# Optimization experiments

Measured on AMD Instinct MI355X. Metric: run time of the kernel, lower is better.

Reference implementation:

```python
import jax, jax.numpy as jnp
import numpy as np

E = 200000     # number of edge-level cells
NADJ = 3200000 # directed up / down adjacency entries (avg degree 16)
F = 64         # input feature dim (== hidden so all layers share dims)
H = 64         # hidden dim
L = 3          # num_layers
B = 64         # number of graphs in batch
C = 10         # num_classes


def setup_inputs() -> dict:
    key = jax.random.key(0)
    ks = jax.random.split(key, 12)
    x = jax.random.normal(ks[0], (E, F), dtype=jnp.float32)
    up_index = jax.random.randint(ks[1], (2, NADJ), 0, E, dtype=jnp.int32)
    up_orient = 2.0 * jax.random.randint(ks[2], (NADJ,), 0, 2).astype(jnp.float32) - 1.0
    down_index = jax.random.randint(ks[3], (2, NADJ), 0, E, dtype=jnp.int32)
    down_orient = 2.0 * jax.random.randint(ks[4], (NADJ,), 0, 2).astype(jnp.float32) - 1.0
    batch = jnp.sort(jax.random.randint(ks[5], (E,), 0, B, dtype=jnp.int32))
    s = 1.0 / np.sqrt(H)
    W_up = jax.random.uniform(ks[6], (L, H, H), minval=-s, maxval=s, dtype=jnp.float32)
    W_down = jax.random.uniform(ks[7], (L, H, H), minval=-s, maxval=s, dtype=jnp.float32)
    W_self = jax.random.uniform(ks[8], (L, H, H), minval=-s, maxval=s, dtype=jnp.float32)
    lin1_w = jax.random.uniform(ks[9], (H, H), minval=-s, maxval=s, dtype=jnp.float32)
    lin1_b = jnp.zeros((H,), jnp.float32)
    lin2_w = jax.random.uniform(ks[10], (C, H), minval=-s, maxval=s, dtype=jnp.float32)
    lin2_b = jnp.zeros((C,), jnp.float32)
    return {"x": x, "up_index": up_index, "up_orient": up_orient,
            "down_index": down_index, "down_orient": down_orient, "batch": batch,
            "W_up": W_up, "W_down": W_down, "W_self": W_self,
            "lin1_w": lin1_w, "lin1_b": lin1_b, "lin2_w": lin2_w, "lin2_b": lin2_b}


def reference(x, up_index, up_orient, down_index, down_orient, batch,
              W_up, W_down, W_self, lin1_w, lin1_b, lin2_w, lin2_b):
    up_src, up_dst = up_index[0], up_index[1]      # message flows src -> dst
    dn_src, dn_dst = down_index[0], down_index[1]
    h = x
    for l in range(L):
        # sign-weighted gather + scatter-sum over upper/lower adjacency
        m_up = jax.ops.segment_sum(h[up_src] * up_orient[:, None], up_dst, num_segments=E)
        m_dn = jax.ops.segment_sum(h[dn_src] * down_orient[:, None], dn_dst, num_segments=E)
        # OrientedConv: act(update_nn(x) + update_up_nn(agg_up) + update_down_nn(agg_down))
        h = jnp.tanh(h @ W_self[l].T + m_up @ W_up[l].T + m_dn @ W_down[l].T)
    # orientation-invariant readout: abs then per-graph segment sum
    pooled = jax.ops.segment_sum(jnp.abs(h), batch, num_segments=B)  # [B, H]
    z = jax.nn.relu(pooled @ lin1_w.T + lin1_b)
    # dropout(p=0.0, eval) is identity
    return z @ lin2_w.T + lin2_b  # [B, C]
```

## Files before the change

kernel.cpp:

```cpp
#include <hip/hip_runtime.h>
#include <hip/hip_bf16.h>

#define H64 64
typedef float float4a __attribute__((ext_vector_type(4)));
typedef float f32x4  __attribute__((ext_vector_type(4)));
typedef short bf16x8 __attribute__((ext_vector_type(8)));

__device__ __forceinline__ unsigned short f2bf(float x) {
    unsigned b = __float_as_uint(x);
    unsigned r = (b + 0x7fffu + ((b >> 16) & 1u)) >> 16;
    return (unsigned short)r;
}

#define SCAN_B 256

#define RPB       512
#define RPB_SH    9
#define NBKT_MAX  1024
#define R1_CHUNK  8192
#define BC_CHUNK  16384

__global__ __launch_bounds__(256) void bcount_kernel(
    const int* __restrict__ up_dst, const int* __restrict__ dn_dst,
    int* __restrict__ bktcnt, int nadj, int E, int nbkt)
{
    __shared__ int lc[NBKT_MAX];
    int t = threadIdx.x;
    for (int i = t; i < nbkt; i += 256) lc[i] = 0;
    __syncthreads();
    long long base = (long long)blockIdx.x * BC_CHUNK;
    long long total = 2LL * nadj;
    for (int i = 0; i < BC_CHUNK / 256; ++i) {
        long long g = base + i * 256 + t;
        if (g < total) {
            int dst2 = (g < nadj) ? up_dst[(int)g] : E + dn_dst[(int)(g - nadj)];
            atomicAdd(&lc[dst2 >> RPB_SH], 1);
        }
    }
    __syncthreads();
    for (int i = t; i < nbkt; i += 256) {
        int c = lc[i];
        if (c) atomicAdd(&bktcnt[i], c);
    }
}

__global__ __launch_bounds__(256) void bscan_kernel(
    const int* __restrict__ bktcnt, int* __restrict__ bstart, int* __restrict__ gcur,
    int nbkt, int total)
{
    __shared__ int s[SCAN_B];
    int t = threadIdx.x;
    int i0 = t * 4;
    int v0 = (i0     < nbkt) ? bktcnt[i0]     : 0;
    int v1 = (i0 + 1 < nbkt) ? bktcnt[i0 + 1] : 0;
    int v2 = (i0 + 2 < nbkt) ? bktcnt[i0 + 2] : 0;
    int v3 = (i0 + 3 < nbkt) ? bktcnt[i0 + 3] : 0;
    int tsum = v0 + v1 + v2 + v3;
    s[t] = tsum; __syncthreads();
    for (int off = 1; off < SCAN_B; off <<= 1) {
        int add = (t >= off) ? s[t - off] : 0;
        int cur = s[t];
        __syncthreads();
        s[t] = cur + add;
        __syncthreads();
    }
    int excl = s[t] - tsum;
    if (i0     < nbkt) { bstart[i0]     = excl;                gcur[i0]     = excl; }
    if (i0 + 1 < nbkt) { bstart[i0 + 1] = excl + v0;           gcur[i0 + 1] = excl + v0; }
    if (i0 + 2 < nbkt) { bstart[i0 + 2] = excl + v0 + v1;      gcur[i0 + 2] = excl + v0 + v1; }
    if (i0 + 3 < nbkt) { bstart[i0 + 3] = excl + v0 + v1 + v2; gcur[i0 + 3] = excl + v0 + v1 + v2; }
    if (t == 0) bstart[nbkt] = total;
}

__global__ __launch_bounds__(256) void bin_kernel(
    const int* __restrict__ up_index, const float* __restrict__ up_orient,
    const int* __restrict__ dn_index, const float* __restrict__ dn_orient,
    int* __restrict__ gcur, unsigned* __restrict__ binned,
    int nadj, int E, int nbkt)
{
    __shared__ unsigned sval[R1_CHUNK];
    __shared__ unsigned short sbkt[R1_CHUNK];
    __shared__ int lcnt[NBKT_MAX];
    __shared__ int goff[NBKT_MAX];
    __shared__ int lrank[NBKT_MAX];

    int t = threadIdx.x;
    for (int b = t; b < nbkt; b += 256) lcnt[b] = 0;
    __syncthreads();

    long long base = (long long)blockIdx.x * R1_CHUNK;
    int total = 2 * nadj;
    #pragma unroll 4
    for (int i = 0; i < R1_CHUNK / 256; ++i) {
        long long g = base + i * 256 + t;
        int li = i * 256 + t;
        if (g < total) {
            int src, dst2; float orient;
            if (g < nadj) {
                int e = (int)g;
                src = up_index[e]; dst2 = up_index[nadj + e]; orient = up_orient[e];
            } else {
                int e = (int)(g - nadj);
                src = dn_index[e]; dst2 = E + dn_index[nadj + e]; orient = dn_orient[e];
            }
            unsigned v = ((unsigned)src << RPB_SH) | (unsigned)(dst2 & (RPB - 1))
                       | (orient < 0.f ? 0x80000000u : 0u);
            int bk = dst2 >> RPB_SH;
            sval[li] = v;
            sbkt[li] = (unsigned short)bk;
            atomicAdd(&lcnt[bk], 1);
        } else {
            sbkt[li] = 0xFFFFu;
        }
    }
    __syncthreads();
    for (int b = t; b < nbkt; b += 256) {
        int c = lcnt[b];
        lrank[b] = 0;
        if (c > 0) goff[b] = atomicAdd(&gcur[b], c);
    }
    __syncthreads();
    #pragma unroll 4
    for (int i = 0; i < R1_CHUNK / 256; ++i) {
        int li = i * 256 + t;
        unsigned short bk = sbkt[li];
        if (bk != 0xFFFFu) {
            int r = atomicAdd(&lrank[bk], 1);
            binned[goff[bk] + r] = sval[li];
        }
    }
}

__global__ __launch_bounds__(256) void csr_fill2_kernel(
    const unsigned* __restrict__ binned, const int* __restrict__ bstart,
    int* __restrict__ end2, unsigned* __restrict__ packed2, int n2)
{
    __shared__ int lh[RPB];
    __shared__ int lcur[RPB];
    __shared__ int s[SCAN_B];
    int b = blockIdx.x;
    int t = threadIdx.x;
    int s0 = bstart[b], s1 = bstart[b + 1];
    int dbase = b << RPB_SH;

    for (int i = t; i < RPB; i += 256) lh[i] = 0;
    __syncthreads();
    for (int i = s0 + t; i < s1; i += 256) {
        unsigned v = binned[i];
        atomicAdd(&lh[v & (RPB - 1)], 1);
    }
    __syncthreads();

    int i0 = t * 2;
    int c0 = lh[i0], c1 = lh[i0 + 1];
    int tsum = c0 + c1;
    s[t] = tsum; __syncthreads();
    for (int off = 1; off < SCAN_B; off <<= 1) {
        int add = (t >= off) ? s[t - off] : 0;
        int cur = s[t];
        __syncthreads();
        s[t] = cur + add;
        __syncthreads();
    }
    int excl = s[t] - tsum;
    lcur[i0]     = excl;
    lcur[i0 + 1] = excl + c0;
    int gd = dbase + i0;
    if (gd     < n2) end2[gd]     = s0 + excl + c0;
    if (gd + 1 < n2) end2[gd + 1] = s0 + excl + tsum;
    __syncthreads();

    for (int i = s0 + t; i < s1; i += 256) {
        unsigned v = binned[i];
        int d = (int)(v & (RPB - 1));
        int p = atomicAdd(&lcur[d], 1);
        packed2[s0 + p] = (v & 0x80000000u) | ((v >> RPB_SH) & 0x1FFFFFu);
    }
}

#define SCAN_TILE 1024

__global__ __launch_bounds__(256) void hist2_kernel(
    const int* __restrict__ up_dst, const int* __restrict__ dn_dst,
    int* __restrict__ deg2, int nadj, int E)
{
    int g = blockIdx.x * 256 + threadIdx.x;
    if (g < nadj) {
        atomicAdd(&deg2[up_dst[g]], 1);
    } else {
        int e = g - nadj;
        if (e < nadj) atomicAdd(&deg2[E + dn_dst[e]], 1);
    }
}

__global__ __launch_bounds__(256) void scan_partial(
    const int* __restrict__ deg, int* __restrict__ bsums, int n)
{
    __shared__ int s[SCAN_B];
    int t = threadIdx.x;
    int i0 = blockIdx.x * SCAN_TILE + t * 4;
    int sum = 0;
    if (i0 + 3 < n) {
        int4 v = *(const int4*)(deg + i0);
        sum = v.x + v.y + v.z + v.w;
    } else {
        for (int k = 0; k < 4; ++k) if (i0 + k < n) sum += deg[i0 + k];
    }
    s[t] = sum; __syncthreads();
    for (int off = 128; off > 0; off >>= 1) {
        if (t < off) s[t] += s[t + off];
        __syncthreads();
    }
    if (t == 0) bsums[blockIdx.x] = s[0];
}

__global__ __launch_bounds__(256) void scan_bsums_k(int* bsums, int nblk)
{
    __shared__ int s[SCAN_B];
    int t = threadIdx.x;
    int i0 = t * 4;
    int v0 = 0, v1 = 0, v2 = 0, v3 = 0;
    if (i0     < nblk) v0 = bsums[i0];
    if (i0 + 1 < nblk) v1 = bsums[i0 + 1];
    if (i0 + 2 < nblk) v2 = bsums[i0 + 2];
    if (i0 + 3 < nblk) v3 = bsums[i0 + 3];
    int tsum = v0 + v1 + v2 + v3;
    s[t] = tsum; __syncthreads();
    for (int off = 1; off < SCAN_B; off <<= 1) {
        int add = (t >= off) ? s[t - off] : 0;
        int cur = s[t];
        __syncthreads();
        s[t] = cur + add;
        __syncthreads();
    }
    int excl = s[t] - tsum;
    if (i0     < nblk) bsums[i0]     = excl;
    if (i0 + 1 < nblk) bsums[i0 + 1] = excl + v0;
    if (i0 + 2 < nblk) bsums[i0 + 2] = excl + v0 + v1;
    if (i0 + 3 < nblk) bsums[i0 + 3] = excl + v0 + v1 + v2;
}

__global__ __launch_bounds__(256) void scan_final(
    const int* __restrict__ deg, const int* __restrict__ bsums,
    int* __restrict__ outx, int n)
{
    __shared__ int s[SCAN_B];
    int t = threadIdx.x;
    int i0 = blockIdx.x * SCAN_TILE + t * 4;
    int v0 = 0, v1 = 0, v2 = 0, v3 = 0;
    if (i0 + 3 < n) {
        int4 v = *(const int4*)(deg + i0);
        v0 = v.x; v1 = v.y; v2 = v.z; v3 = v.w;
    } else {
        if (i0     < n) v0 = deg[i0];
        if (i0 + 1 < n) v1 = deg[i0 + 1];
        if (i0 + 2 < n) v2 = deg[i0 + 2];
        if (i0 + 3 < n) v3 = deg[i0 + 3];
    }
    int tsum = v0 + v1 + v2 + v3;
    s[t] = tsum; __syncthreads();
    for (int off = 1; off < SCAN_B; off <<= 1) {
        int add = (t >= off) ? s[t - off] : 0;
        int cur = s[t];
        __syncthreads();
        s[t] = cur + add;
        __syncthreads();
    }
    int excl = s[t] - tsum;
    int base = bsums[blockIdx.x] + excl;
    if (i0     < n) outx[i0]     = base;
    if (i0 + 1 < n) outx[i0 + 1] = base + v0;
    if (i0 + 2 < n) outx[i0 + 2] = base + v0 + v1;
    if (i0 + 3 < n) outx[i0 + 3] = base + v0 + v1 + v2;
}

__global__ __launch_bounds__(256) void reorder2_kernel(
    const int* __restrict__ up_index, const float* __restrict__ up_orient,
    const int* __restrict__ dn_index, const float* __restrict__ dn_orient,
    int* __restrict__ end2, unsigned* __restrict__ packed2, int nadj, int E)
{
    int g = blockIdx.x * 256 + threadIdx.x;
    if (g < nadj) {
        int src = up_index[g];
        int dst = up_index[nadj + g];
        int p = atomicAdd(&end2[dst], 1);
        packed2[p] = (unsigned)src | (up_orient[g] < 0.f ? 0x80000000u : 0u);
    } else {
        int e = g - nadj;
        if (e < nadj) {
            int src = dn_index[e];
            int dst = dn_index[nadj + e];
            int p = atomicAdd(&end2[E + dst], 1);
            packed2[p] = (unsigned)src | (dn_orient[e] < 0.f ? 0x80000000u : 0u);
        }
    }
}

__global__ __launch_bounds__(256) void conv_bf16_kernel(
    const float* __restrict__ x, unsigned short* __restrict__ hb, size_t n)
{
    size_t i = ((size_t)blockIdx.x * 256 + threadIdx.x) * 4;
    if (i + 3 < n) {
        float4a v = *(const float4a*)(x + i);
        uint2 o;
        o.x = (unsigned)f2bf(v[0]) | ((unsigned)f2bf(v[1]) << 16);
        o.y = (unsigned)f2bf(v[2]) | ((unsigned)f2bf(v[3]) << 16);
        *(uint2*)(hb + i) = o;
    } else {
        for (size_t k = i; k < n; ++k) hb[k] = f2bf(x[k]);
    }
}

__global__ __launch_bounds__(256) void convW_kernel(
    const float* __restrict__ Ws, const float* __restrict__ Wu,
    const float* __restrict__ Wd, unsigned short* __restrict__ Wb, int L)
{
    int i = blockIdx.x * 256 + threadIdx.x;
    int total = L * 3 * 4096;
    if (i >= total) return;
    int l = i / (3 * 4096);
    int m = (i / 4096) % 3;
    int r = i & 4095;
    const float* src = (m == 0) ? Ws : ((m == 1) ? Wu : Wd);
    Wb[i] = f2bf(src[l * 4096 + r]);
}

__device__ __forceinline__ void seg_sum2_slow(
    const unsigned* __restrict__ hb32, const unsigned* __restrict__ packed2,
    int s0, int s1, unsigned fp, int g, int lane, float& r0, float& r1)
{
    float a0 = 0.f, a1 = 0.f;
    for (int b = s0; b < s1; b += 64) {
        int cnt = min(64, s1 - b);
        unsigned pk = (lane < cnt) ? packed2[b + lane] : 0u;
        for (int n = 0; n < cnt; n += 2) {
            int idx = n + g;
            unsigned pe = __shfl(pk, min(idx, cnt - 1));
            float sgn = (idx < cnt) ? (((int)pe < 0) ? -1.f : 1.f) : 0.f;
            unsigned u = hb32[(pe << 5) + fp];
            a0 = fmaf(__uint_as_float(u << 16),         sgn, a0);
            a1 = fmaf(__uint_as_float(u & 0xFFFF0000u), sgn, a1);
        }
    }
    r0 = a0; r1 = a1;
}

__global__ __launch_bounds__(256) void gather_kernel(
    const unsigned* __restrict__ hb32,
    const int* __restrict__ end2, const unsigned* __restrict__ packed2,
    unsigned* __restrict__ mup32, unsigned* __restrict__ mdn32, int E)
{
    int dst = (int)((blockIdx.x * 256u + threadIdx.x) >> 6);
    if (dst >= E) return;
    int lane = threadIdx.x & 63;
    int g  = lane >> 5;
    unsigned fp = lane & 31;

    int s0U = (dst == 0) ? 0 : end2[dst - 1];
    int s1U = end2[dst];
    int s0D = end2[E + dst - 1];
    int s1D = end2[E + dst];
    int cntU = s1U - s0U, cntD = s1D - s0D;

    float u0, u1, d0, d1;
    if (cntU <= 64 && cntD <= 64) {
        int limU = max(cntU - 1, 0), limD = max(cntD - 1, 0);
        unsigned pkU = (cntU > 0) ? packed2[s0U + min(lane, limU)] : 0u;
        unsigned pkD = (cntD > 0) ? packed2[s0D + min(lane, limD)] : 0u;
        float a0 = 0.f, a1 = 0.f, b0 = 0.f, b1 = 0.f;
        int nmax = max(cntU, cntD);
        for (int n = 0; n < nmax; n += 8) {
            unsigned pU[4], pD[4], vU[4], vD[4];
            float sU[4], sD[4];
            #pragma unroll
            for (int t = 0; t < 4; ++t) {
                int idx = n + 2 * t + g;
                pU[t] = __shfl(pkU, min(idx, limU));
                pD[t] = __shfl(pkD, min(idx, limD));
                sU[t] = (idx < cntU) ? (((int)pU[t] < 0) ? -1.f : 1.f) : 0.f;
                sD[t] = (idx < cntD) ? (((int)pD[t] < 0) ? -1.f : 1.f) : 0.f;
            }
            #pragma unroll
            for (int t = 0; t < 4; ++t) vU[t] = hb32[(pU[t] << 5) + fp];
            #pragma unroll
            for (int t = 0; t < 4; ++t) vD[t] = hb32[(pD[t] << 5) + fp];
            #pragma unroll
            for (int t = 0; t < 4; ++t) {
                a0 = fmaf(__uint_as_float(vU[t] << 16),         sU[t], a0);
                a1 = fmaf(__uint_as_float(vU[t] & 0xFFFF0000u), sU[t], a1);
                b0 = fmaf(__uint_as_float(vD[t] << 16),         sD[t], b0);
                b1 = fmaf(__uint_as_float(vD[t] & 0xFFFF0000u), sD[t], b1);
            }
        }
        u0 = a0; u1 = a1; d0 = b0; d1 = b1;
    } else {
        seg_sum2_slow(hb32, packed2, s0U, s1U, fp, g, lane, u0, u1);
        seg_sum2_slow(hb32, packed2, s0D, s1D, fp, g, lane, d0, d1);
    }

    u0 += __shfl_xor(u0, 32); u1 += __shfl_xor(u1, 32);
    d0 += __shfl_xor(d0, 32); d1 += __shfl_xor(d1, 32);

    unsigned valU = (unsigned)f2bf(u0) | ((unsigned)f2bf(u1) << 16);
    unsigned valD = (unsigned)f2bf(d0) | ((unsigned)f2bf(d1) << 16);
    unsigned* ptr = g ? mdn32 : mup32;
    ptr[(size_t)dst * 32 + fp] = g ? valD : valU;
}

__global__ __launch_bounds__(256) void gemm_tanh_mfma(
    const unsigned short* __restrict__ hbin,
    const unsigned short* __restrict__ mupb, const unsigned short* __restrict__ mdnb,
    const unsigned short* __restrict__ Wb,
    unsigned short* __restrict__ hbout, int E, int nblk16)
{
    int wid  = (blockIdx.x * 256 + threadIdx.x) >> 6;
    if (wid >= nblk16) return;
    int lane = threadIdx.x & 63;
    int lg = lane >> 4;
    int lr = lane & 15;

    bf16x8 bfr[3][4][2];
    #pragma unroll
    for (int m = 0; m < 3; ++m)
        #pragma unroll
        for (int jt = 0; jt < 4; ++jt)
            #pragma unroll
            for (int ks = 0; ks < 2; ++ks)
                bfr[m][jt][ks] = *(const bf16x8*)(Wb + m * 4096 + (jt * 16 + lr) * 64 + ks * 32 + lg * 8);

    int base = wid * 16;
    int arow = base + lr;
    bool ok = (arow < E);
    size_t aoff = (size_t)arow * H64 + lg * 8;

    bf16x8 afr[3][2];
    bf16x8 zz = {0, 0, 0, 0, 0, 0, 0, 0};
    #pragma unroll
    for (int ks = 0; ks < 2; ++ks) {
        afr[0][ks] = ok ? *(const bf16x8*)(hbin + aoff + ks * 32) : zz;
        afr[1][ks] = ok ? *(const bf16x8*)(mupb + aoff + ks * 32) : zz;
        afr[2][ks] = ok ? *(const bf16x8*)(mdnb + aoff + ks * 32) : zz;
    }

    f32x4 acc[4];
    #pragma unroll
    for (int jt = 0; jt < 4; ++jt) acc[jt] = (f32x4){0.f, 0.f, 0.f, 0.f};

    #pragma unroll
    for (int m = 0; m < 3; ++m)
        #pragma unroll
        for (int ks = 0; ks < 2; ++ks)
            #pragma unroll
            for (int jt = 0; jt < 4; ++jt)
                acc[jt] = __builtin_amdgcn_mfma_f32_16x16x32_bf16(
                    afr[m][ks], bfr[m][jt][ks], acc[jt], 0, 0, 0);

    #pragma unroll
    for (int jt = 0; jt < 4; ++jt) {
        #pragma unroll
        for (int reg = 0; reg < 4; ++reg) {
            int row = base + lg * 4 + reg;
            if (row < E) {
                float v = acc[jt][reg];
                float e2 = __expf(2.f * v);
                float val = 1.f - 2.f / (e2 + 1.f);
                hbout[(size_t)row * H64 + jt * 16 + lr] = f2bf(val);
            }
        }
    }
}

#define ROWS_PER_WAVE 64
__global__ __launch_bounds__(256) void pool_kernel(
    const unsigned short* __restrict__ hb, const int* __restrict__ batch,
    float* __restrict__ pooled, int E)
{
    int wave = (int)((blockIdx.x * 256 + threadIdx.x) >> 6);
    int j = threadIdx.x & 63;
    int row0 = wave * ROWS_PER_WAVE;
    if (row0 >= E) return;
    int row1 = min(row0 + ROWS_PER_WAVE, E);

    int cur = batch[row0];
    float acc = 0.f;
    for (int i = row0; i < row1; ++i) {
        int b = batch[i];
        if (b != cur) {
            atomicAdd(&pooled[(size_t)cur * H64 + j], acc);
            acc = 0.f;
            cur = b;
        }
        unsigned u = hb[(size_t)i * H64 + j];
        acc += fabsf(__uint_as_float(u << 16));
    }
    atomicAdd(&pooled[(size_t)cur * H64 + j], acc);
}

__global__ __launch_bounds__(64) void head_kernel(
    const float* __restrict__ pooled,
    const float* __restrict__ lin1_w, const float* __restrict__ lin1_b,
    const float* __restrict__ lin2_w, const float* __restrict__ lin2_b,
    float* __restrict__ out, int C)
{
    __shared__ float p[64];
    __shared__ float z[64];
    int b = blockIdx.x;
    int t = threadIdx.x;

    p[t] = pooled[(size_t)b * H64 + t];
    __syncthreads();

    float acc = lin1_b[t];
    #pragma unroll
    for (int k = 0; k < 64; ++k) acc += p[k] * lin1_w[t * 64 + k];
    z[t] = fmaxf(acc, 0.f);
    __syncthreads();

    if (t < C) {
        float o = lin2_b[t];
        #pragma unroll
        for (int k = 0; k < 64; ++k) o += z[k] * lin2_w[t * 64 + k];
        out[(size_t)b * C + t] = o;
    }
}

extern "C" void kernel_launch(void* const* d_in, const int* in_sizes, int n_in,
                              void* d_out, int out_size, void* d_ws, size_t ws_size,
                              hipStream_t stream)
{
    const float* x          = (const float*)d_in[0];
    const int*   up_index   = (const int*)  d_in[1];
    const float* up_orient  = (const float*)d_in[2];
    const int*   down_index = (const int*)  d_in[3];
    const float* down_orient= (const float*)d_in[4];
    const int*   batch      = (const int*)  d_in[5];
    const float* W_up       = (const float*)d_in[6];
    const float* W_down     = (const float*)d_in[7];
    const float* W_self     = (const float*)d_in[8];
    const float* lin1_w     = (const float*)d_in[9];
    const float* lin1_b     = (const float*)d_in[10];
    const float* lin2_w     = (const float*)d_in[11];
    const float* lin2_b     = (const float*)d_in[12];
    float* out = (float*)d_out;

    const int E    = in_sizes[0] / H64;
    const int NADJ = in_sizes[1] / 2;
    const int C    = in_sizes[11] / H64;
    const int B    = out_size / C;
    const int L    = in_sizes[6] / (H64 * H64);

    unsigned short* hb      = (unsigned short*)d_ws;
    unsigned short* mupb    = hb   + (size_t)E * H64;
    unsigned short* mdnb    = mupb + (size_t)E * H64;
    float*          pooled  = (float*)(mdnb + (size_t)E * H64);
    int*            end2    = (int*)(pooled + (size_t)B * H64);
    int*            deg2    = end2 + (size_t)2 * E;
    int*            bsums   = deg2 + (size_t)2 * E;
    int*            bktcnt  = bsums + 1024;
    int*            gcur    = bktcnt + NBKT_MAX;
    int*            bstart  = gcur + NBKT_MAX;
    unsigned short* Wb      = (unsigned short*)(bstart + NBKT_MAX + 1);
    unsigned*       packed2 = (unsigned*)(Wb + (size_t)L * 3 * 4096);
    unsigned*       binned  = packed2 + (size_t)2 * NADJ;

    const int n2    = 2 * E;
    const int nbkt  = (n2 + RPB - 1) >> RPB_SH;
    const int total = 2 * NADJ;
    const int gather_blocks = (int)(((long long)E * 64 + 255) / 256);
    const int conv_blocks   = (int)(((long long)E * H64 / 4 + 255) / 256);
    const int nblk16        = (E + 15) / 16;
    const int gemm_blocks   = (nblk16 + 3) / 4;
    const int convw_blocks  = (L * 3 * 4096 + 255) / 256;
    const int pool_waves    = (E + ROWS_PER_WAVE - 1) / ROWS_PER_WAVE;
    const int pool_blocks   = (pool_waves + 3) / 4;

    if (nbkt <= NBKT_MAX) {
        const int bc_blocks = (total + BC_CHUNK - 1) / BC_CHUNK;
        const int r1_blocks = (total + R1_CHUNK - 1) / R1_CHUNK;
        hipMemsetAsync(bktcnt, 0, (size_t)NBKT_MAX * sizeof(int), stream);
        bcount_kernel<<<bc_blocks, 256, 0, stream>>>(up_index + NADJ, down_index + NADJ,
                                                     bktcnt, NADJ, E, nbkt);
        bscan_kernel<<<1, 256, 0, stream>>>(bktcnt, bstart, gcur, nbkt, total);
        bin_kernel<<<r1_blocks, 256, 0, stream>>>(up_index, up_orient, down_index, down_orient,
                                                  gcur, binned, NADJ, E, nbkt);
        csr_fill2_kernel<<<nbkt, 256, 0, stream>>>(binned, bstart, end2, packed2, n2);
    } else {
        const int both_blocks = (total + 255) / 256;
        const int nscan = (n2 + SCAN_TILE - 1) / SCAN_TILE;
        hipMemsetAsync(deg2, 0, (size_t)n2 * sizeof(int), stream);
        hist2_kernel<<<both_blocks, 256, 0, stream>>>(up_index + NADJ, down_index + NADJ, deg2, NADJ, E);
        scan_partial<<<nscan, 256, 0, stream>>>(deg2, bsums, n2);
        scan_bsums_k<<<1, 256, 0, stream>>>(bsums, nscan);
        scan_final<<<nscan, 256, 0, stream>>>(deg2, bsums, end2, n2);
        reorder2_kernel<<<both_blocks, 256, 0, stream>>>(up_index, up_orient, down_index, down_orient,
                                                         end2, packed2, NADJ, E);
    }

    conv_bf16_kernel<<<conv_blocks, 256, 0, stream>>>(x, hb, (size_t)E * H64);
    convW_kernel<<<convw_blocks, 256, 0, stream>>>(W_self, W_up, W_down, Wb, L);

    for (int l = 0; l < L; ++l) {
        gather_kernel<<<gather_blocks, 256, 0, stream>>>(
            (const unsigned*)hb, end2, packed2,
            (unsigned*)mupb, (unsigned*)mdnb, E);
        gemm_tanh_mfma<<<gemm_blocks, 256, 0, stream>>>(
            hb, mupb, mdnb, Wb + (size_t)l * 3 * 4096, hb, E, nblk16);
    }

    hipMemsetAsync(pooled, 0, (size_t)B * H64 * sizeof(float), stream);
    pool_kernel<<<pool_blocks, 256, 0, stream>>>(hb, batch, pooled, E);
    head_kernel<<<B, 64, 0, stream>>>(pooled, lin1_w, lin1_b, lin2_w, lin2_b, out, C);
}
```

Baseline: 731.5 us.

## Fuse conversion kernels, split gather tail loops, stream GEMM weight loads

Merges the activation and weight bf16 conversion kernels into one launch, saving a kernel launch. The gather loop now runs paired up/down iterations only up to the smaller count and finishes the rest in separate single-direction loops, so the direction with fewer neighbours no longer issues wasted clamped loads. The MFMA GEMM loads the A and B fragments per matrix inside the loop instead of preloading all of them into registers, which lowers register pressure and may raise occupancy but puts the weight loads closer to their use.

```diff
diff --git a/kernel.cpp b/kernel.cpp
--- a/kernel.cpp
+++ b/kernel.cpp
@@ -296,33 +296,33 @@
     }
 }
 
-__global__ __launch_bounds__(256) void conv_bf16_kernel(
-    const float* __restrict__ x, unsigned short* __restrict__ hb, size_t n)
-{
-    size_t i = ((size_t)blockIdx.x * 256 + threadIdx.x) * 4;
-    if (i + 3 < n) {
-        float4a v = *(const float4a*)(x + i);
-        uint2 o;
-        o.x = (unsigned)f2bf(v[0]) | ((unsigned)f2bf(v[1]) << 16);
-        o.y = (unsigned)f2bf(v[2]) | ((unsigned)f2bf(v[3]) << 16);
-        *(uint2*)(hb + i) = o;
-    } else {
-        for (size_t k = i; k < n; ++k) hb[k] = f2bf(x[k]);
-    }
-}
-
-__global__ __launch_bounds__(256) void convW_kernel(
+__global__ __launch_bounds__(256) void conv_all_kernel(
+    const float* __restrict__ x, unsigned short* __restrict__ hb, size_t n,
+    int conv_blocks,
     const float* __restrict__ Ws, const float* __restrict__ Wu,
     const float* __restrict__ Wd, unsigned short* __restrict__ Wb, int L)
 {
-    int i = blockIdx.x * 256 + threadIdx.x;
-    int total = L * 3 * 4096;
-    if (i >= total) return;
-    int l = i / (3 * 4096);
-    int m = (i / 4096) % 3;
-    int r = i & 4095;
-    const float* src = (m == 0) ? Ws : ((m == 1) ? Wu : Wd);
-    Wb[i] = f2bf(src[l * 4096 + r]);
+    if (blockIdx.x < (unsigned)conv_blocks) {
+        size_t i = ((size_t)blockIdx.x * 256 + threadIdx.x) * 4;
+        if (i + 3 < n) {
+            float4a v = *(const float4a*)(x + i);
+            uint2 o;
+            o.x = (unsigned)f2bf(v[0]) | ((unsigned)f2bf(v[1]) << 16);
+            o.y = (unsigned)f2bf(v[2]) | ((unsigned)f2bf(v[3]) << 16);
+            *(uint2*)(hb + i) = o;
+        } else {
+            for (size_t k = i; k < n; ++k) hb[k] = f2bf(x[k]);
+        }
+    } else {
+        int i = (blockIdx.x - conv_blocks) * 256 + threadIdx.x;
+        int total = L * 3 * 4096;
+        if (i >= total) return;
+        int l = i / (3 * 4096);
+        int m = (i / 4096) % 3;
+        int r = i & 4095;
+        const float* src = (m == 0) ? Ws : ((m == 1) ? Wu : Wd);
+        Wb[i] = f2bf(src[l * 4096 + r]);
+    }
 }
 
 __device__ __forceinline__ void seg_sum2_slow(
@@ -368,8 +368,9 @@
         unsigned pkU = (cntU > 0) ? packed2[s0U + min(lane, limU)] : 0u;
         unsigned pkD = (cntD > 0) ? packed2[s0D + min(lane, limD)] : 0u;
         float a0 = 0.f, a1 = 0.f, b0 = 0.f, b1 = 0.f;
-        int nmax = max(cntU, cntD);
-        for (int n = 0; n < nmax; n += 8) {
+        int nmin = min(cntU, cntD);
+        int n = 0;
+        for (; n < nmin; n += 8) {
             unsigned pU[4], pD[4], vU[4], vD[4];
             float sU[4], sD[4];
             #pragma unroll
@@ -392,6 +393,38 @@
                 b1 = fmaf(__uint_as_float(vD[t] & 0xFFFF0000u), sD[t], b1);
             }
         }
+        for (int q = n; q < cntU; q += 8) {
+            unsigned p[4], v[4]; float sg[4];
+            #pragma unroll
+            for (int t = 0; t < 4; ++t) {
+                int idx = q + 2 * t + g;
+                p[t] = __shfl(pkU, min(idx, limU));
+                sg[t] = (idx < cntU) ? (((int)p[t] < 0) ? -1.f : 1.f) : 0.f;
+            }
+            #pragma unroll
+            for (int t = 0; t < 4; ++t) v[t] = hb32[(p[t] << 5) + fp];
+            #pragma unroll
+            for (int t = 0; t < 4; ++t) {
+                a0 = fmaf(__uint_as_float(v[t] << 16),         sg[t], a0);
+                a1 = fmaf(__uint_as_float(v[t] & 0xFFFF0000u), sg[t], a1);
+            }
+        }
+        for (int q = n; q < cntD; q += 8) {
+            unsigned p[4], v[4]; float sg[4];
+            #pragma unroll
+            for (int t = 0; t < 4; ++t) {
+                int idx = q + 2 * t + g;
+                p[t] = __shfl(pkD, min(idx, limD));
+                sg[t] = (idx < cntD) ? (((int)p[t] < 0) ? -1.f : 1.f) : 0.f;
+            }
+            #pragma unroll
+            for (int t = 0; t < 4; ++t) v[t] = hb32[(p[t] << 5) + fp];
+            #pragma unroll
+            for (int t = 0; t < 4; ++t) {
+                b0 = fmaf(__uint_as_float(v[t] << 16),         sg[t], b0);
+                b1 = fmaf(__uint_as_float(v[t] & 0xFFFF0000u), sg[t], b1);
+            }
+        }
         u0 = a0; u1 = a1; d0 = b0; d1 = b1;
     } else {
         seg_sum2_slow(hb32, packed2, s0U, s1U, fp, g, lane, u0, u1);
@@ -419,41 +452,30 @@
     int lg = lane >> 4;
     int lr = lane & 15;
 
-    bf16x8 bfr[3][4][2];
-    #pragma unroll
-    for (int m = 0; m < 3; ++m)
-        #pragma unroll
-        for (int jt = 0; jt < 4; ++jt)
-            #pragma unroll
-            for (int ks = 0; ks < 2; ++ks)
-                bfr[m][jt][ks] = *(const bf16x8*)(Wb + m * 4096 + (jt * 16 + lr) * 64 + ks * 32 + lg * 8);
-
     int base = wid * 16;
     int arow = base + lr;
     bool ok = (arow < E);
     size_t aoff = (size_t)arow * H64 + lg * 8;
 
-    bf16x8 afr[3][2];
-    bf16x8 zz = {0, 0, 0, 0, 0, 0, 0, 0};
-    #pragma unroll
-    for (int ks = 0; ks < 2; ++ks) {
-        afr[0][ks] = ok ? *(const bf16x8*)(hbin + aoff + ks * 32) : zz;
-        afr[1][ks] = ok ? *(const bf16x8*)(mupb + aoff + ks * 32) : zz;
-        afr[2][ks] = ok ? *(const bf16x8*)(mdnb + aoff + ks * 32) : zz;
-    }
-
     f32x4 acc[4];
     #pragma unroll
     for (int jt = 0; jt < 4; ++jt) acc[jt] = (f32x4){0.f, 0.f, 0.f, 0.f};
 
+    bf16x8 zz = {0, 0, 0, 0, 0, 0, 0, 0};
     #pragma unroll
-    for (int m = 0; m < 3; ++m)
+    for (int m = 0; m < 3; ++m) {
+        const unsigned short* src = (m == 0) ? hbin : ((m == 1) ? mupb : mdnb);
+        bf16x8 a0 = ok ? *(const bf16x8*)(src + aoff)      : zz;
+        bf16x8 a1 = ok ? *(const bf16x8*)(src + aoff + 32) : zz;
+        const unsigned short* wbase = Wb + m * 4096 + lr * 64 + lg * 8;
         #pragma unroll
-        for (int ks = 0; ks < 2; ++ks)
-            #pragma unroll
-            for (int jt = 0; jt < 4; ++jt)
-                acc[jt] = __builtin_amdgcn_mfma_f32_16x16x32_bf16(
-                    afr[m][ks], bfr[m][jt][ks], acc[jt], 0, 0, 0);
+        for (int jt = 0; jt < 4; ++jt) {
+            bf16x8 b0 = *(const bf16x8*)(wbase + jt * 1024);
+            bf16x8 b1 = *(const bf16x8*)(wbase + jt * 1024 + 32);
+            acc[jt] = __builtin_amdgcn_mfma_f32_16x16x32_bf16(a0, b0, acc[jt], 0, 0, 0);
+            acc[jt] = __builtin_amdgcn_mfma_f32_16x16x32_bf16(a1, b1, acc[jt], 0, 0, 0);
+        }
+    }
 
     #pragma unroll
     for (int jt = 0; jt < 4; ++jt) {
@@ -568,9 +590,9 @@
     const int total = 2 * NADJ;
     const int gather_blocks = (int)(((long long)E * 64 + 255) / 256);
     const int conv_blocks   = (int)(((long long)E * H64 / 4 + 255) / 256);
+    const int convw_blocks  = (L * 3 * 4096 + 255) / 256;
     const int nblk16        = (E + 15) / 16;
     const int gemm_blocks   = (nblk16 + 3) / 4;
-    const int convw_blocks  = (L * 3 * 4096 + 255) / 256;
     const int pool_waves    = (E + ROWS_PER_WAVE - 1) / ROWS_PER_WAVE;
     const int pool_blocks   = (pool_waves + 3) / 4;
 
@@ -596,8 +618,8 @@
                                                          end2, packed2, NADJ, E);
     }
 
-    conv_bf16_kernel<<<conv_blocks, 256, 0, stream>>>(x, hb, (size_t)E * H64);
-    convW_kernel<<<convw_blocks, 256, 0, stream>>>(W_self, W_up, W_down, Wb, L);
+    conv_all_kernel<<<conv_blocks + convw_blocks, 256, 0, stream>>>(
+        x, hb, (size_t)E * H64, conv_blocks, W_self, W_up, W_down, Wb, L);
 
     for (int l = 0; l < L; ++l) {
         gather_kernel<<<gather_blocks, 256, 0, stream>>>(
```

Result: faster. 713.8 us (-2.4%).
